# Kernel optimization log

Hardware: AMD Instinct MI355X
Metric: run time of the kernel (lower is better)

Reference implementation:

```python
import jax, jax.numpy as jnp
import numpy as np

MAX_DISP = 4          # 9x9 displacement window -> 81 output channels
WIN = 2 * MAX_DISP + 1


def setup_inputs() -> dict:
    key = jax.random.key(0)
    k1, k2 = jax.random.split(key)
    B, C, H, W = 4, 256, 192, 192
    tensorFirst = jax.random.normal(k1, (B, C, H, W), dtype=jnp.float32)
    tensorSecond = jax.random.normal(k2, (B, C, H, W), dtype=jnp.float32)
    return {"tensorFirst": tensorFirst, "tensorSecond": tensorSecond}


def reference(tensorFirst, tensorSecond):
    # PWC-Net correlation: out[b, (dy+4)*9+(dx+4), y, x] =
    #   mean_c first[b,c,y,x] * second[b,c,y+dy,x+dx]  (second zero-padded by 4)
    B, C, H, W = tensorFirst.shape
    padded = jnp.pad(tensorSecond, ((0, 0), (0, 0), (MAX_DISP, MAX_DISP), (MAX_DISP, MAX_DISP)))
    outs = []
    for dy in range(WIN):
        for dx in range(WIN):
            shifted = padded[:, :, dy:dy + H, dx:dx + W]  # [B,C,H,W]
            outs.append(jnp.mean(tensorFirst * shifted, axis=1))  # [B,H,W]
    return jnp.stack(outs, axis=1)  # [B,81,H,W]
```

## Files before the change

### kernel.cpp

```cpp
#include <hip/hip_runtime.h>


#define MAXD 4
#define WINW 9
#define NDISP 81

constexpr int B_ = 4, C_ = 256, H_ = 192, W_ = 192;
constexpr int TH = 4;
constexpr int TW = 64;
constexpr int CC = 4;
constexpr int NCHUNK = C_ / CC;
constexpr int SROWS = TH + 2 * MAXD;
constexpr int SCOLS = TW + 2 * MAXD;
constexpr int F_STRIDE = 68;
constexpr int S_STRIDE = 72;
constexpr int F_CH = TH * F_STRIDE;
constexpr int S_CH = SROWS * S_STRIDE;
constexpr int FBUF = CC * F_CH;
constexpr int SBUF = CC * S_CH;
constexpr int NTHREADS = 576;
constexpr int NF4 = CC * TH * (TW / 4);
constexpr int NS4 = CC * SROWS * (SCOLS / 4);

__global__ __launch_bounds__(NTHREADS)
void corr_kernel(const float* __restrict__ F, const float* __restrict__ S,
                 float* __restrict__ O) {
    __shared__ __align__(16) float ldsF[2 * FBUF];
    __shared__ __align__(16) float ldsS[2 * SBUF];

    const int tid  = threadIdx.x;
    const int y0   = blockIdx.x * TH;
    const int x0   = blockIdx.y * TW;
    const int b    = blockIdx.z;
    const int dy   = tid >> 6;
    const int lane = tid & 63;
    const int xg   = lane & 15;
    const int yth  = lane >> 4;

    const long planeHW  = (long)H_ * W_;
    const long chunkStep = (long)CC * planeHW;
    const float* Fb = F + (long)b * C_ * planeHW;
    const float* Sb = S + (long)b * C_ * planeHW;

    const bool fAct = (tid < NF4);
    const int  fcc  = tid >> 6;
    const int  fyr  = (tid >> 4) & 3;
    const int  fcg  = tid & 15;
    const int  fLds = fcc * F_CH + fyr * F_STRIDE + 4 * fcg;
    const float* fPtr0 = Fb + (long)fcc * planeHW + (long)(y0 + fyr) * W_ + (x0 + 4 * fcg);

    const int  s0cc  = tid / (SROWS * (SCOLS / 4));
    const int  s0rem = tid - s0cc * (SROWS * (SCOLS / 4));
    const int  s0r   = s0rem / (SCOLS / 4);
    const int  s0cg  = s0rem - s0r * (SCOLS / 4);
    const int  s0ys  = y0 - MAXD + s0r;
    const int  s0xs  = x0 - MAXD + 4 * s0cg;
    const bool s0In  = ((unsigned)s0ys < (unsigned)H_) &&
                       ((unsigned)s0xs <= (unsigned)(W_ - 4));
    const int  s0Lds = s0cc * S_CH + s0r * S_STRIDE + 4 * s0cg;
    const float* s0Ptr0 = Sb + (long)s0cc * planeHW + (long)s0ys * W_ + s0xs;

    const int  i1    = tid + NTHREADS;
    const bool s1Act = (i1 < NS4);
    const int  s1cc  = i1 / (SROWS * (SCOLS / 4));
    const int  s1rem = i1 - s1cc * (SROWS * (SCOLS / 4));
    const int  s1r   = s1rem / (SCOLS / 4);
    const int  s1cg  = s1rem - s1r * (SCOLS / 4);
    const int  s1ys  = y0 - MAXD + s1r;
    const int  s1xs  = x0 - MAXD + 4 * s1cg;
    const bool s1In  = s1Act && ((unsigned)s1ys < (unsigned)H_) &&
                       ((unsigned)s1xs <= (unsigned)(W_ - 4));
    const int  s1Lds = s1cc * S_CH + s1r * S_STRIDE + 4 * s1cg;
    const float* s1Ptr0 = Sb + (long)s1cc * planeHW + (long)s1ys * W_ + s1xs;

    const float4 z4 = make_float4(0.f, 0.f, 0.f, 0.f);
    if (!s0In) {
        *(float4*)(ldsS + s0Lds) = z4;
        *(float4*)(ldsS + SBUF + s0Lds) = z4;
    }
    if (s1Act && !s1In) {
        *(float4*)(ldsS + s1Lds) = z4;
        *(float4*)(ldsS + SBUF + s1Lds) = z4;
    }

    float4 pf, ps0, ps1;
    const float* fNext  = fPtr0;
    const float* s0Next = s0Ptr0;
    const float* s1Next = s1Ptr0;

    auto loadRegs = [&]() {
        if (fAct) pf  = *(const float4*)fNext;
        if (s0In) ps0 = *(const float4*)s0Next;
        if (s1In) ps1 = *(const float4*)s1Next;
        fNext  += chunkStep;
        s0Next += chunkStep;
        s1Next += chunkStep;
    };

    auto writeLds = [&](int half) {
        float* wF = ldsF + half * FBUF;
        float* wS = ldsS + half * SBUF;
        if (fAct) *(float4*)(wF + fLds)  = pf;
        if (s0In) *(float4*)(wS + s0Lds) = ps0;
        if (s1In) *(float4*)(wS + s1Lds) = ps1;
    };

    float acc[WINW][4];
    #pragma unroll
    for (int dx = 0; dx < WINW; ++dx)
        #pragma unroll
        for (int j = 0; j < 4; ++j) acc[dx][j] = 0.f;

    auto computeChunk = [&](int half) {
        const float* bF = ldsF + half * FBUF + yth * F_STRIDE + 4 * xg;
        const float* bS = ldsS + half * SBUF + (yth + dy) * S_STRIDE + 4 * xg;
        #pragma unroll
        for (int cc = 0; cc < CC; ++cc) {
            const float4 f  = *(const float4*)(bF + cc * F_CH);
            const float4 w0 = *(const float4*)(bS + cc * S_CH);
            const float4 w1 = *(const float4*)(bS + cc * S_CH + 4);
            const float4 w2 = *(const float4*)(bS + cc * S_CH + 8);
            const float w[12] = {w0.x, w0.y, w0.z, w0.w,
                                 w1.x, w1.y, w1.z, w1.w,
                                 w2.x, w2.y, w2.z, w2.w};
            #pragma unroll
            for (int dx = 0; dx < WINW; ++dx) {
                acc[dx][0] += f.x * w[dx];
                acc[dx][1] += f.y * w[dx + 1];
                acc[dx][2] += f.z * w[dx + 2];
                acc[dx][3] += f.w * w[dx + 3];
            }
        }
    };

    loadRegs();
    writeLds(0);
    loadRegs();
    __syncthreads();

    for (int k = 0; k < NCHUNK; ++k) {
        const int cur = k & 1;
        computeChunk(cur);
        if (k + 1 < NCHUNK) {
            writeLds(cur ^ 1);
            if (k + 2 < NCHUNK) loadRegs();
            __syncthreads();
        }
    }

    const float scale = 1.0f / (float)C_;
    #pragma unroll
    for (int dx = 0; dx < WINW; ++dx) {
        float4 o;
        o.x = acc[dx][0] * scale;
        o.y = acc[dx][1] * scale;
        o.z = acc[dx][2] * scale;
        o.w = acc[dx][3] * scale;
        const int d = dy * WINW + dx;
        float* dst = O + ((long)(b * NDISP + d) * H_ + (y0 + yth)) * W_ + x0 + 4 * xg;
        *(float4*)dst = o;
    }
}

extern "C" void kernel_launch(void* const* d_in, const int* in_sizes, int n_in,
                              void* d_out, int out_size, void* d_ws, size_t ws_size,
                              hipStream_t stream) {
    const float* F = (const float*)d_in[0];
    const float* S = (const float*)d_in[1];
    float* O = (float*)d_out;
    dim3 grid(H_ / TH, W_ / TW, B_);
    dim3 block(NTHREADS);
    corr_kernel<<<grid, block, 0, stream>>>(F, S, O);
}
```

Measured before the change: 413.8 us.

## Split channel reduction across four blocks with atomic accumulation; load F directly to registers

Splits the 256-channel reduction into four slices handled by separate blocks, which quadruples the grid. Partial sums are combined with float atomicAdd into an output that is first zeroed by a memset. The First tensor is now read straight from global memory into registers instead of being staged through LDS, which removes that LDS buffer and its writes. The trade-offs are four times as many atomic writes to the 81-channel output, an extra memset, and a sum order that is no longer deterministic.

After: 893.5 us. 2.16x slower.

```diff
diff --git a/kernel.cpp b/kernel.cpp
--- a/kernel.cpp
+++ b/kernel.cpp
@@ -8,46 +8,40 @@
 constexpr int B_ = 4, C_ = 256, H_ = 192, W_ = 192;
 constexpr int TH = 4;
 constexpr int TW = 64;
+constexpr int CSPLIT = 4;
+constexpr int CPB = C_ / CSPLIT;
 constexpr int CC = 4;
-constexpr int NCHUNK = C_ / CC;
+constexpr int NCHUNK = CPB / CC;
 constexpr int SROWS = TH + 2 * MAXD;
 constexpr int SCOLS = TW + 2 * MAXD;
-constexpr int F_STRIDE = 68;
 constexpr int S_STRIDE = 72;
-constexpr int F_CH = TH * F_STRIDE;
 constexpr int S_CH = SROWS * S_STRIDE;
-constexpr int FBUF = CC * F_CH;
 constexpr int SBUF = CC * S_CH;
 constexpr int NTHREADS = 576;
-constexpr int NF4 = CC * TH * (TW / 4);
 constexpr int NS4 = CC * SROWS * (SCOLS / 4);
 
 __global__ __launch_bounds__(NTHREADS)
 void corr_kernel(const float* __restrict__ F, const float* __restrict__ S,
                  float* __restrict__ O) {
-    __shared__ __align__(16) float ldsF[2 * FBUF];
     __shared__ __align__(16) float ldsS[2 * SBUF];
 
     const int tid  = threadIdx.x;
     const int y0   = blockIdx.x * TH;
     const int x0   = blockIdx.y * TW;
-    const int b    = blockIdx.z;
+    const int zb   = blockIdx.z;
+    const int b    = zb >> 2;
+    const int cq   = zb & 3;
     const int dy   = tid >> 6;
     const int lane = tid & 63;
     const int xg   = lane & 15;
     const int yth  = lane >> 4;
 
-    const long planeHW  = (long)H_ * W_;
+    const long planeHW   = (long)H_ * W_;
     const long chunkStep = (long)CC * planeHW;
-    const float* Fb = F + (long)b * C_ * planeHW;
-    const float* Sb = S + (long)b * C_ * planeHW;
+    const float* Fb = F + ((long)b * C_ + cq * CPB) * planeHW;
+    const float* Sb = S + ((long)b * C_ + cq * CPB) * planeHW;
 
-    const bool fAct = (tid < NF4);
-    const int  fcc  = tid >> 6;
-    const int  fyr  = (tid >> 4) & 3;
-    const int  fcg  = tid & 15;
-    const int  fLds = fcc * F_CH + fyr * F_STRIDE + 4 * fcg;
-    const float* fPtr0 = Fb + (long)fcc * planeHW + (long)(y0 + fyr) * W_ + (x0 + 4 * fcg);
+    const float* fp = Fb + (long)(y0 + yth) * W_ + (x0 + 4 * xg);
 
     const int  s0cc  = tid / (SROWS * (SCOLS / 4));
     const int  s0rem = tid - s0cc * (SROWS * (SCOLS / 4));
@@ -83,24 +77,18 @@
         *(float4*)(ldsS + SBUF + s1Lds) = z4;
     }
 
-    float4 pf, ps0, ps1;
-    const float* fNext  = fPtr0;
+    float4 ps0, ps1;
     const float* s0Next = s0Ptr0;
     const float* s1Next = s1Ptr0;
 
-    auto loadRegs = [&]() {
-        if (fAct) pf  = *(const float4*)fNext;
+    auto loadS = [&]() {
         if (s0In) ps0 = *(const float4*)s0Next;
         if (s1In) ps1 = *(const float4*)s1Next;
-        fNext  += chunkStep;
         s0Next += chunkStep;
         s1Next += chunkStep;
     };
-
-    auto writeLds = [&](int half) {
-        float* wF = ldsF + half * FBUF;
+    auto writeS = [&](int half) {
         float* wS = ldsS + half * SBUF;
-        if (fAct) *(float4*)(wF + fLds)  = pf;
         if (s0In) *(float4*)(wS + s0Lds) = ps0;
         if (s1In) *(float4*)(wS + s1Lds) = ps1;
     };
@@ -111,12 +99,30 @@
         #pragma unroll
         for (int j = 0; j < 4; ++j) acc[dx][j] = 0.f;
 
-    auto computeChunk = [&](int half) {
-        const float* bF = ldsF + half * FBUF + yth * F_STRIDE + 4 * xg;
-        const float* bS = ldsS + half * SBUF + (yth + dy) * S_STRIDE + 4 * xg;
+    loadS();
+    writeS(0);
+    loadS();
+    __syncthreads();
+
+    const float* bS0 = ldsS + (yth + dy) * S_STRIDE + 4 * xg;
+
+    for (int k = 0; k < NCHUNK; ++k) {
+        float4 fr[CC];
+        #pragma unroll
+        for (int cc = 0; cc < CC; ++cc)
+            fr[cc] = *(const float4*)(fp + (long)cc * planeHW);
+        fp += chunkStep;
+
+        const int cur = k & 1;
+        if (k + 1 < NCHUNK) {
+            writeS(cur ^ 1);
+            if (k + 2 < NCHUNK) loadS();
+        }
+
+        const float* bS = bS0 + cur * SBUF;
         #pragma unroll
         for (int cc = 0; cc < CC; ++cc) {
-            const float4 f  = *(const float4*)(bF + cc * F_CH);
+            const float4 f  = fr[cc];
             const float4 w0 = *(const float4*)(bS + cc * S_CH);
             const float4 w1 = *(const float4*)(bS + cc * S_CH + 4);
             const float4 w2 = *(const float4*)(bS + cc * S_CH + 8);
@@ -131,34 +137,19 @@
                 acc[dx][3] += f.w * w[dx + 3];
             }
         }
-    };
 
-    loadRegs();
-    writeLds(0);
-    loadRegs();
-    __syncthreads();
-
-    for (int k = 0; k < NCHUNK; ++k) {
-        const int cur = k & 1;
-        computeChunk(cur);
-        if (k + 1 < NCHUNK) {
-            writeLds(cur ^ 1);
-            if (k + 2 < NCHUNK) loadRegs();
-            __syncthreads();
-        }
+        if (k + 1 < NCHUNK) __syncthreads();
     }
 
     const float scale = 1.0f / (float)C_;
     #pragma unroll
     for (int dx = 0; dx < WINW; ++dx) {
-        float4 o;
-        o.x = acc[dx][0] * scale;
-        o.y = acc[dx][1] * scale;
-        o.z = acc[dx][2] * scale;
-        o.w = acc[dx][3] * scale;
         const int d = dy * WINW + dx;
         float* dst = O + ((long)(b * NDISP + d) * H_ + (y0 + yth)) * W_ + x0 + 4 * xg;
-        *(float4*)dst = o;
+        atomicAdd(dst + 0, acc[dx][0] * scale);
+        atomicAdd(dst + 1, acc[dx][1] * scale);
+        atomicAdd(dst + 2, acc[dx][2] * scale);
+        atomicAdd(dst + 3, acc[dx][3] * scale);
     }
 }
 
@@ -168,7 +159,8 @@
     const float* F = (const float*)d_in[0];
     const float* S = (const float*)d_in[1];
     float* O = (float*)d_out;
-    dim3 grid(H_ / TH, W_ / TW, B_);
+    hipMemsetAsync(d_out, 0, (size_t)out_size, stream);
+    dim3 grid(H_ / TH, W_ / TW, B_ * CSPLIT);
     dim3 block(NTHREADS);
     corr_kernel<<<grid, block, 0, stream>>>(F, S, O);
 }
```
